# Kernel optimization log

Measured on AMD Instinct MI355X. Metric: run time of the kernel, lower is better.

Reference implementation:

```python
import jax, jax.numpy as jnp
import numpy as np


def setup_inputs() -> dict:
    key = jax.random.key(0)
    k1, k2 = jax.random.split(key)
    B, C, H, W = 32, 64, 64, 64
    K = 512
    z_e = jax.random.normal(k1, (B, C, H, W), dtype=jnp.float32)
    # codebook initialized uniform(-1/K, 1/K) as in the torch module
    codebook = jax.random.uniform(k2, (K, C), dtype=jnp.float32,
                                  minval=-1.0 / K, maxval=1.0 / K)
    return {"z_e": z_e, "codebook": codebook}


def reference(z_e, codebook):
    B, C, H, W = z_e.shape
    commitment_cost = 0.25
    # [B*H*W, C]
    z_flat = jnp.transpose(z_e, (0, 2, 3, 1)).reshape(-1, C)
    dists = (jnp.sum(z_flat * z_flat, axis=1, keepdims=True)
             + jnp.sum(codebook * codebook, axis=1)
             - 2.0 * jnp.matmul(z_flat, codebook.T))
    encoding_indices = jnp.argmin(dists, axis=1)  # [N] int
    z_q = codebook[encoding_indices].reshape(B, H, W, C)
    z_q = jnp.transpose(z_q, (0, 3, 1, 2))  # [B, C, H, W]
    q_loss = jnp.mean((z_q - jax.lax.stop_gradient(z_e)) ** 2)
    e_loss = jnp.mean((z_e - jax.lax.stop_gradient(z_q)) ** 2)
    loss = q_loss + commitment_cost * e_loss
    # straight-through estimator
    z_q_st = z_e + jax.lax.stop_gradient(z_q - z_e)
    return (z_q_st, encoding_indices, loss)
```

## Files before the change

### kernel.cpp

```cpp
#include <hip/hip_runtime.h>
#include <cfloat>

typedef __attribute__((ext_vector_type(8))) short short8;
typedef __attribute__((ext_vector_type(4))) float f32x4;

constexpr int C_DIM    = 64;
constexpr int K_CODES  = 512;
constexpr int HW       = 4096;
constexpr int CHW      = 262144;
constexpr int NPTS     = 131072;
constexpr int ZQ_SIZE  = 8388608;
constexpr int IDX_OFF  = ZQ_SIZE;
constexpr int LOSS_OFF = ZQ_SIZE + NPTS;
constexpr int TILE     = 128;
constexpr int CHUNK    = 256;
constexpr int NSLOT    = 16;
constexpr size_t WS_BF16 = (size_t)K_CODES * C_DIM * 2;
constexpr size_t WS_NEED = WS_BF16 + (size_t)K_CODES * 4;

__device__ __forceinline__ unsigned short f32_to_bf16_rne(float f) {
    unsigned u = __float_as_uint(f);
    unsigned r = u + 0x7fffu + ((u >> 16) & 1u);
    return (unsigned short)(r >> 16);
}

template <int STRIDE>
__device__ __forceinline__ float np_sumsq64(const float* __restrict__ a) {
    float r[8];
#pragma unroll
    for (int j = 0; j < 8; ++j) { const float v = a[j * STRIDE]; r[j] = __fmul_rn(v, v); }
#pragma unroll
    for (int i = 8; i < 64; i += 8)
#pragma unroll
        for (int j = 0; j < 8; ++j) {
            const float v = a[(i + j) * STRIDE];
            r[j] = __fadd_rn(r[j], __fmul_rn(v, v));
        }
    return __fadd_rn(
        __fadd_rn(__fadd_rn(r[0], r[1]), __fadd_rn(r[2], r[3])),
        __fadd_rn(__fadd_rn(r[4], r[5]), __fadd_rn(r[6], r[7])));
}

__global__ void vq_zero(float* __restrict__ out) { out[LOSS_OFF] = 0.0f; }

__global__ void vq_prep(const float* __restrict__ cb, unsigned short* __restrict__ wsb,
                        float* __restrict__ wsB, float* __restrict__ out) {
    const int gid = blockIdx.x * 256 + threadIdx.x;
    wsb[gid] = f32_to_bf16_rne(cb[gid]);
    if (gid < K_CODES) wsB[gid] = np_sumsq64<1>(cb + gid * C_DIM);
    if (gid == 0) out[LOSS_OFF] = 0.0f;
}

__global__ __launch_bounds__(256, 4) void vq_idx(const float* __restrict__ ze,
                                                 const float* __restrict__ cb,
                                                 float* __restrict__ out,
                                                 const unsigned short* __restrict__ wsb,
                                                 const float* __restrict__ wsB,
                                                 int use_ws)
{
    __shared__ unsigned short eh[CHUNK * C_DIM];
    __shared__ float  BsL[K_CODES];
    __shared__ float  As[TILE];
    __shared__ unsigned short cand[TILE * NSLOT];
    __shared__ int    cnt[TILE];
    __shared__ int    bestk[TILE];
    __shared__ double lred[4];

    const int tid  = threadIdx.x;
    const int lane = tid & 63, w = tid >> 6;
    const int quad = lane >> 4, l15 = lane & 15;
    const int n0   = blockIdx.x * TILE;
    const int b    = n0 >> 12, hw0 = n0 & (HW - 1);
    const float* zebase = ze + b * CHW + hw0;

    if (use_ws) { for (int k = tid; k < K_CODES; k += 256) BsL[k] = wsB[k]; }
    else        { for (int k = tid; k < K_CODES; k += 256) BsL[k] = np_sumsq64<1>(cb + k * C_DIM); }
    if (tid < TILE) { As[tid] = np_sumsq64<HW>(zebase + tid); cnt[tid] = 0; }
    __syncthreads();

    short8 afr[2][2];
    float  A_pt[2][4], thr[2][4], runmin[2][4];
#pragma unroll
    for (int rt = 0; rt < 2; ++rt) {
        const int pt = w * 32 + rt * 16 + l15;
#pragma unroll
        for (int kc = 0; kc < 2; ++kc) {
            union { unsigned short s[8]; short8 v; } u;
#pragma unroll
            for (int j = 0; j < 8; ++j) {
                const int c = kc * 32 + quad * 8 + j;
                u.s[j] = f32_to_bf16_rne(zebase[c * HW + pt]);
            }
            afr[rt][kc] = u.v;
        }
#pragma unroll
        for (int r = 0; r < 4; ++r) {
            A_pt[rt][r]   = As[w * 32 + rt * 16 + quad * 4 + r];
            runmin[rt][r] = FLT_MAX;
        }
    }

    auto stage = [&](int ch) {
        const int row = tid;
        uint4* base = (uint4*)eh;
        if (use_ws) {
            const uint4* src = (const uint4*)(wsb + (size_t)(ch * CHUNK + row) * C_DIM);
#pragma unroll
            for (int s = 0; s < 8; ++s) base[row * 8 + (s ^ (row & 7))] = src[s];
        } else {
            const float4* src = (const float4*)(cb + (size_t)(ch * CHUNK + row) * C_DIM);
#pragma unroll
            for (int s = 0; s < 8; ++s) {
                const float4 f0 = src[2 * s], f1 = src[2 * s + 1];
                uint4 o;
                o.x = (unsigned)f32_to_bf16_rne(f0.x) | ((unsigned)f32_to_bf16_rne(f0.y) << 16);
                o.y = (unsigned)f32_to_bf16_rne(f0.z) | ((unsigned)f32_to_bf16_rne(f0.w) << 16);
                o.z = (unsigned)f32_to_bf16_rne(f1.x) | ((unsigned)f32_to_bf16_rne(f1.y) << 16);
                o.w = (unsigned)f32_to_bf16_rne(f1.z) | ((unsigned)f32_to_bf16_rne(f1.w) << 16);
                base[row * 8 + (s ^ (row & 7))] = o;
            }
        }
    };

    for (int ch = 0; ch < 2; ++ch) {
        __syncthreads(); stage(ch); __syncthreads();
        const uint4* ebase = (const uint4*)eh;
#pragma unroll 4
        for (int tile = 0; tile < 16; ++tile) {
            const int cl = tile * 16 + l15;
            const short8 b0 = *(const short8*)&ebase[cl * 8 + ((quad    ) ^ (cl & 7))];
            const short8 b1 = *(const short8*)&ebase[cl * 8 + ((quad + 4) ^ (cl & 7))];
            const float bs = BsL[ch * CHUNK + cl];
#pragma unroll
            for (int rt = 0; rt < 2; ++rt) {
                f32x4 acc = {0.f, 0.f, 0.f, 0.f};
                acc = __builtin_amdgcn_mfma_f32_16x16x32_bf16(afr[rt][0], b0, acc, 0, 0, 0);
                acc = __builtin_amdgcn_mfma_f32_16x16x32_bf16(afr[rt][1], b1, acc, 0, 0, 0);
#pragma unroll
                for (int r = 0; r < 4; ++r) {
                    const float D = fmaf(-2.f, acc[r], __fadd_rn(A_pt[rt][r], bs));
                    runmin[rt][r] = fminf(runmin[rt][r], D);
                }
            }
        }
    }
#pragma unroll
    for (int rt = 0; rt < 2; ++rt)
#pragma unroll
        for (int r = 0; r < 4; ++r) {
            float v = runmin[rt][r];
#pragma unroll
            for (int m = 1; m < 16; m <<= 1) v = fminf(v, __shfl_xor(v, m, 64));
            thr[rt][r] = v + (4e-4f * sqrtf(A_pt[rt][r]) + 3e-4f);
        }

    auto scan_push = [&](int ch) {
        const uint4* ebase = (const uint4*)eh;
#pragma unroll 4
        for (int tile = 0; tile < 16; ++tile) {
            const int cl = tile * 16 + l15;
            const short8 b0 = *(const short8*)&ebase[cl * 8 + ((quad    ) ^ (cl & 7))];
            const short8 b1 = *(const short8*)&ebase[cl * 8 + ((quad + 4) ^ (cl & 7))];
            const float bs = BsL[ch * CHUNK + cl];
#pragma unroll
            for (int rt = 0; rt < 2; ++rt) {
                f32x4 acc = {0.f, 0.f, 0.f, 0.f};
                acc = __builtin_amdgcn_mfma_f32_16x16x32_bf16(afr[rt][0], b0, acc, 0, 0, 0);
                acc = __builtin_amdgcn_mfma_f32_16x16x32_bf16(afr[rt][1], b1, acc, 0, 0, 0);
#pragma unroll
                for (int r = 0; r < 4; ++r) {
                    const float D = fmaf(-2.f, acc[r], __fadd_rn(A_pt[rt][r], bs));
                    if (D <= thr[rt][r]) {
                        const int pt = w * 32 + rt * 16 + quad * 4 + r;
                        const int p = atomicAdd(&cnt[pt], 1);
                        if (p < NSLOT) cand[pt * NSLOT + p] = (unsigned short)(ch * CHUNK + cl);
                    }
                }
            }
        }
    };
    scan_push(1);
    __syncthreads(); stage(0); __syncthreads();
    scan_push(0);
    __syncthreads();

    if (tid < TILE) {
        const int c = cnt[tid];
        if (c <= NSLOT) {
            const float Av = As[tid];
            float bD = FLT_MAX; int bK = K_CODES;
            for (int i = 0; i < c; ++i) {
                const int k = cand[tid * NSLOT + i];
                const float* er = cb + k * C_DIM;
                float M = 0.f;
#pragma unroll
                for (int cc = 0; cc < 64; ++cc) M = fmaf(zebase[cc * HW + tid], er[cc], M);
                const float D = fmaf(-2.f, M, __fadd_rn(Av, BsL[k]));
                if (D < bD || (D == bD && k < bK)) { bD = D; bK = k; }
            }
            bestk[tid] = bK;
            out[IDX_OFF + n0 + tid] = (float)bK;
        }
    }
    __syncthreads();

    for (int pp = 0; pp < 32; ++pp) {
        const int pt = w * 32 + pp;
        if (cnt[pt] <= NSLOT) continue;
        const float Av = As[pt];
        float bD = FLT_MAX; int bK = K_CODES;
        for (int k = lane; k < K_CODES; k += 64) {
            const float* er = cb + k * C_DIM;
            float M = 0.f;
#pragma unroll
            for (int cc = 0; cc < 64; ++cc) M = fmaf(zebase[cc * HW + pt], er[cc], M);
            const float D = fmaf(-2.f, M, __fadd_rn(Av, BsL[k]));
            if (D < bD || (D == bD && k < bK)) { bD = D; bK = k; }
        }
#pragma unroll
        for (int off = 1; off < 64; off <<= 1) {
            const float oD = __shfl_xor(bD, off, 64);
            const int   oK = __shfl_xor(bK, off, 64);
            if (oD < bD || (oD == bD && oK < bK)) { bD = oD; bK = oK; }
        }
        if (lane == 0) { bestk[pt] = bK; out[IDX_OFF + n0 + pt] = (float)bK; }
    }
    __syncthreads();

    double ls = 0.0;
#pragma unroll
    for (int it = 0; it < 8; ++it) {
        const int task = tid + 256 * it;
        const int c = task >> 5, q = task & 31;
        const float4 xz = *(const float4*)(zebase + c * HW + 4 * q);
        float o[4];
#pragma unroll
        for (int j = 0; j < 4; ++j) {
            const int k = bestk[4 * q + j];
            const float ev = cb[k * C_DIM + c];
            const float xv = (j == 0) ? xz.x : (j == 1) ? xz.y : (j == 2) ? xz.z : xz.w;
            const float d = __fsub_rn(ev, xv);
            o[j] = __fadd_rn(xv, d);
            ls = fma((double)d, (double)d, ls);
        }
        *(float4*)(out + b * CHW + c * HW + hw0 + 4 * q) = make_float4(o[0], o[1], o[2], o[3]);
    }
#pragma unroll
    for (int off = 32; off > 0; off >>= 1) ls += __shfl_xor(ls, off, 64);
    if ((tid & 63) == 0) lred[w] = ls;
    __syncthreads();
    if (tid == 0)
        atomicAdd(out + LOSS_OFF,
                  (float)((lred[0] + lred[1] + lred[2] + lred[3]) * (1.25 / (double)ZQ_SIZE)));
}

extern "C" void kernel_launch(void* const* d_in, const int* in_sizes, int n_in,
                              void* d_out, int out_size, void* d_ws, size_t ws_size,
                              hipStream_t stream) {
    (void)in_sizes; (void)n_in; (void)out_size;
    const float* ze = (const float*)d_in[0];
    const float* cb = (const float*)d_in[1];
    float* out = (float*)d_out;
    const int use_ws = (ws_size >= WS_NEED) ? 1 : 0;
    unsigned short* wsb = (unsigned short*)d_ws;
    float* wsB = (float*)((char*)d_ws + WS_BF16);

    if (use_ws) vq_prep<<<(K_CODES * C_DIM) / 256, 256, 0, stream>>>(cb, wsb, wsB, out);
    else        vq_zero<<<1, 1, 0, stream>>>(out);
    vq_idx<<<NPTS / TILE, 256, 0, stream>>>(ze, cb, out, wsb, wsB, use_ws);
}
```

Measured before the change: 141.7 us.

## Cache z_e tile in shared memory and stage codebook in smaller chunks

Loads the 64x128 z_e tile once into padded shared memory with coalesced float4 reads and reuses it for the norm, the bf16 MFMA fragments, the exact rescoring and the output pass, instead of issuing strided global reads each time. Codebook staging drops from 256-row to 64-row chunks, which shrinks LDS use (likely to let more blocks fit per CU) at the cost of many more block barriers. The candidate rescoring is also split across two threads per point with a shuffle merge.

```diff
diff --git a/kernel.cpp b/kernel.cpp
--- a/kernel.cpp
+++ b/kernel.cpp
@@ -13,8 +13,9 @@
 constexpr int IDX_OFF  = ZQ_SIZE;
 constexpr int LOSS_OFF = ZQ_SIZE + NPTS;
 constexpr int TILE     = 128;
-constexpr int CHUNK    = 256;
+constexpr int CHUNK    = 64;
 constexpr int NSLOT    = 16;
+constexpr int ZP       = TILE + 4;
 constexpr size_t WS_BF16 = (size_t)K_CODES * C_DIM * 2;
 constexpr size_t WS_NEED = WS_BF16 + (size_t)K_CODES * 4;
 
@@ -58,6 +59,7 @@
                                                  const float* __restrict__ wsB,
                                                  int use_ws)
 {
+    __shared__ __align__(16) float zeC[C_DIM][ZP];
     __shared__ unsigned short eh[CHUNK * C_DIM];
     __shared__ float  BsL[K_CODES];
     __shared__ float  As[TILE];
@@ -73,44 +75,33 @@
     const int b    = n0 >> 12, hw0 = n0 & (HW - 1);
     const float* zebase = ze + b * CHW + hw0;
 
+#pragma unroll
+    for (int i = 0; i < 8; ++i) {
+        const int idx = tid + 256 * i;
+        const int c = idx >> 5, q = idx & 31;
+        const float4 v = *(const float4*)(zebase + c * HW + 4 * q);
+        *(float4*)&zeC[c][4 * q] = v;
+    }
     if (use_ws) { for (int k = tid; k < K_CODES; k += 256) BsL[k] = wsB[k]; }
     else        { for (int k = tid; k < K_CODES; k += 256) BsL[k] = np_sumsq64<1>(cb + k * C_DIM); }
-    if (tid < TILE) { As[tid] = np_sumsq64<HW>(zebase + tid); cnt[tid] = 0; }
-    __syncthreads();
-
-    short8 afr[2][2];
-    float  A_pt[2][4], thr[2][4], runmin[2][4];
-#pragma unroll
-    for (int rt = 0; rt < 2; ++rt) {
-        const int pt = w * 32 + rt * 16 + l15;
-#pragma unroll
-        for (int kc = 0; kc < 2; ++kc) {
-            union { unsigned short s[8]; short8 v; } u;
-#pragma unroll
-            for (int j = 0; j < 8; ++j) {
-                const int c = kc * 32 + quad * 8 + j;
-                u.s[j] = f32_to_bf16_rne(zebase[c * HW + pt]);
-            }
-            afr[rt][kc] = u.v;
-        }
-#pragma unroll
-        for (int r = 0; r < 4; ++r) {
-            A_pt[rt][r]   = As[w * 32 + rt * 16 + quad * 4 + r];
-            runmin[rt][r] = FLT_MAX;
-        }
-    }
+    if (tid < TILE) cnt[tid] = 0;
+    __syncthreads();
 
     auto stage = [&](int ch) {
-        const int row = tid;
+        const int row = tid >> 2, sl0 = (tid & 3) * 2;
         uint4* base = (uint4*)eh;
         if (use_ws) {
             const uint4* src = (const uint4*)(wsb + (size_t)(ch * CHUNK + row) * C_DIM);
 #pragma unroll
-            for (int s = 0; s < 8; ++s) base[row * 8 + (s ^ (row & 7))] = src[s];
+            for (int t = 0; t < 2; ++t) {
+                const int s = sl0 + t;
+                base[row * 8 + (s ^ (row & 7))] = src[s];
+            }
         } else {
             const float4* src = (const float4*)(cb + (size_t)(ch * CHUNK + row) * C_DIM);
 #pragma unroll
-            for (int s = 0; s < 8; ++s) {
+            for (int t = 0; t < 2; ++t) {
+                const int s = sl0 + t;
                 const float4 f0 = src[2 * s], f1 = src[2 * s + 1];
                 uint4 o;
                 o.x = (unsigned)f32_to_bf16_rne(f0.x) | ((unsigned)f32_to_bf16_rne(f0.y) << 16);
@@ -122,11 +113,36 @@
         }
     };
 
-    for (int ch = 0; ch < 2; ++ch) {
-        __syncthreads(); stage(ch); __syncthreads();
+    if (tid < TILE) As[tid] = np_sumsq64<ZP>(&zeC[0][tid]);
+    stage(0);
+    __syncthreads();
+
+    short8 afr[2][2];
+    float  A_pt[2][4], thr[2][4], runmin[2][4];
+#pragma unroll
+    for (int rt = 0; rt < 2; ++rt) {
+        const int pt = w * 32 + rt * 16 + l15;
+#pragma unroll
+        for (int kc = 0; kc < 2; ++kc) {
+            union { unsigned short s[8]; short8 v; } u;
+#pragma unroll
+            for (int j = 0; j < 8; ++j) {
+                const int c = kc * 32 + quad * 8 + j;
+                u.s[j] = f32_to_bf16_rne(zeC[c][pt]);
+            }
+            afr[rt][kc] = u.v;
+        }
+#pragma unroll
+        for (int r = 0; r < 4; ++r) {
+            A_pt[rt][r]   = As[w * 32 + rt * 16 + quad * 4 + r];
+            runmin[rt][r] = FLT_MAX;
+        }
+    }
+
+    for (int ch = 0; ch < 8; ++ch) {
         const uint4* ebase = (const uint4*)eh;
-#pragma unroll 4
-        for (int tile = 0; tile < 16; ++tile) {
+#pragma unroll
+        for (int tile = 0; tile < 4; ++tile) {
             const int cl = tile * 16 + l15;
             const short8 b0 = *(const short8*)&ebase[cl * 8 + ((quad    ) ^ (cl & 7))];
             const short8 b1 = *(const short8*)&ebase[cl * 8 + ((quad + 4) ^ (cl & 7))];
@@ -143,6 +159,7 @@
                 }
             }
         }
+        if (ch < 7) { __syncthreads(); stage(ch + 1); __syncthreads(); }
     }
 #pragma unroll
     for (int rt = 0; rt < 2; ++rt)
@@ -156,8 +173,8 @@
 
     auto scan_push = [&](int ch) {
         const uint4* ebase = (const uint4*)eh;
-#pragma unroll 4
-        for (int tile = 0; tile < 16; ++tile) {
+#pragma unroll
+        for (int tile = 0; tile < 4; ++tile) {
             const int cl = tile * 16 + l15;
             const short8 b0 = *(const short8*)&ebase[cl * 8 + ((quad    ) ^ (cl & 7))];
             const short8 b1 = *(const short8*)&ebase[cl * 8 + ((quad + 4) ^ (cl & 7))];
@@ -179,27 +196,32 @@
             }
         }
     };
-    scan_push(1);
-    __syncthreads(); stage(0); __syncthreads();
-    scan_push(0);
-    __syncthreads();
-
-    if (tid < TILE) {
-        const int c = cnt[tid];
+    scan_push(7);
+    for (int ch = 0; ch < 7; ++ch) {
+        __syncthreads(); stage(ch); __syncthreads();
+        scan_push(ch);
+    }
+    __syncthreads();
+
+    {
+        const int pt = tid >> 1, j0 = tid & 1;
+        const int c = cnt[pt];
         if (c <= NSLOT) {
-            const float Av = As[tid];
+            const float Av = As[pt];
             float bD = FLT_MAX; int bK = K_CODES;
-            for (int i = 0; i < c; ++i) {
-                const int k = cand[tid * NSLOT + i];
+            for (int i = j0; i < c; i += 2) {
+                const int k = cand[pt * NSLOT + i];
                 const float* er = cb + k * C_DIM;
                 float M = 0.f;
 #pragma unroll
-                for (int cc = 0; cc < 64; ++cc) M = fmaf(zebase[cc * HW + tid], er[cc], M);
+                for (int cc = 0; cc < 64; ++cc) M = fmaf(zeC[cc][pt], er[cc], M);
                 const float D = fmaf(-2.f, M, __fadd_rn(Av, BsL[k]));
                 if (D < bD || (D == bD && k < bK)) { bD = D; bK = k; }
             }
-            bestk[tid] = bK;
-            out[IDX_OFF + n0 + tid] = (float)bK;
+            const float oD = __shfl_xor(bD, 1, 64);
+            const int   oK = __shfl_xor(bK, 1, 64);
+            if (oD < bD || (oD == bD && oK < bK)) { bD = oD; bK = oK; }
+            if (j0 == 0) { bestk[pt] = bK; out[IDX_OFF + n0 + pt] = (float)bK; }
         }
     }
     __syncthreads();
@@ -213,7 +235,7 @@
             const float* er = cb + k * C_DIM;
             float M = 0.f;
 #pragma unroll
-            for (int cc = 0; cc < 64; ++cc) M = fmaf(zebase[cc * HW + pt], er[cc], M);
+            for (int cc = 0; cc < 64; ++cc) M = fmaf(zeC[cc][pt], er[cc], M);
             const float D = fmaf(-2.f, M, __fadd_rn(Av, BsL[k]));
             if (D < bD || (D == bD && k < bK)) { bD = D; bK = k; }
         }
@@ -232,7 +254,7 @@
     for (int it = 0; it < 8; ++it) {
         const int task = tid + 256 * it;
         const int c = task >> 5, q = task & 31;
-        const float4 xz = *(const float4*)(zebase + c * HW + 4 * q);
+        const float4 xz = *(const float4*)&zeC[c][4 * q];
         float o[4];
 #pragma unroll
         for (int j = 0; j < 4; ++j) {
```

After: 163.7 us. 15.5% more time.
